# Kernel tuning notes

Measured on AMD Instinct MI355X. Metric: run time of the kernel, lower is better.

## Reference

```python
import jax, jax.numpy as jnp
import numpy as np

B, VL, TL, KL = 2, 2048, 448, 64  # batch, vision_len, text_len, task_len
H, NH, D = 1024, 16, 64           # hidden, num_heads, head_dim


def _linear(x, w, b):
    # torch nn.Linear convention: w is [out, in]
    return x @ w.T + b


def _attn(q, k, v):
    # q: [b, ql, n, d], k/v: [b, kl, n, d] -> [b, ql, n, d]
    d = q.shape[-1]
    scores = jnp.einsum('bqnd,bknd->bnqk', q, k) / d  # note: /d, not /sqrt(d), as in source
    probs = jax.nn.softmax(scores, axis=-1)
    return jnp.einsum('bnqk,bknd->bqnd', probs, v)


def setup_inputs() -> dict:
    key = jax.random.key(0)
    ks = jax.random.split(key, 20)
    s = 0.02
    inp = {
        'vision_hidden_states': jax.random.normal(ks[0], (B, VL, H), jnp.float32),
        'text_hidden_states': jax.random.normal(ks[1], (B, TL, H), jnp.float32),
        'task_hidden_states': jax.random.normal(ks[2], (B, KL, H), jnp.float32),
        'wq0': jax.random.normal(ks[3], (H, H), jnp.float32) * s,
        'bq0': jnp.zeros((H,), jnp.float32),
        'wk0': jax.random.normal(ks[4], (H, H), jnp.float32) * s,
        'bk0': jnp.zeros((H,), jnp.float32),
        'wv0': jax.random.normal(ks[5], (H, H), jnp.float32) * s,
        'bv0': jnp.zeros((H,), jnp.float32),
        'wq1': jax.random.normal(ks[6], (D, D), jnp.float32) * s,
        'bq1': jnp.zeros((D,), jnp.float32),
        'wk1': jax.random.normal(ks[7], (D, D), jnp.float32) * s,
        'bk1': jnp.zeros((D,), jnp.float32),
        'wv1': jax.random.normal(ks[8], (D, D), jnp.float32) * s,
        'bv1': jnp.zeros((D,), jnp.float32),
        'wo': jax.random.normal(ks[9], (H, H), jnp.float32) * s,
        'bo': jnp.zeros((H,), jnp.float32),
    }
    return inp


def reference(vision_hidden_states, text_hidden_states, task_hidden_states,
              wq0, bq0, wk0, bk0, wv0, bv0,
              wq1, bq1, wk1, bk1, wv1, bv1, wo, bo):
    b, vl, h = vision_hidden_states.shape
    tl = text_hidden_states.shape[1]
    kl = task_hidden_states.shape[1]
    total = vl + tl + kl

    hs = jnp.concatenate([vision_hidden_states, text_hidden_states, task_hidden_states], axis=1)
    q0 = _linear(hs, wq0, bq0).reshape(b, total, NH, D)
    k0 = _linear(hs, wk0, bk0).reshape(b, total, NH, D)
    v0 = _linear(hs, wv0, bv0).reshape(b, total, NH, D)

    vq, tq, kq = q0[:, :vl], q0[:, vl:vl + tl], q0[:, vl + tl:]
    vk, tk, kk = k0[:, :vl], k0[:, vl:vl + tl], k0[:, vl + tl:]
    vv, tv = v0[:, :vl], v0[:, vl:vl + tl]
    kv = q0[:, vl + tl:]  # faithful to source bug: task_v comes from q0

    v2t = _attn(vq, tk, tv)  # vision attends to text: [b, vl, n, d]
    t2v = _attn(tq, vk, vv)  # text attends to vision: [b, tl, n, d]
    mid = jnp.concatenate([v2t, t2v], axis=1)  # [b, vl+tl, n, d]

    q1 = jnp.concatenate([kq, _linear(mid, wq1, bq1)], axis=1)
    k1 = jnp.concatenate([kk, _linear(mid, wk1, bk1)], axis=1)
    v1 = jnp.concatenate([kv, _linear(mid, wv1, bv1)], axis=1)

    out = _attn(q1, k1, v1).reshape(b, total, NH * D)
    return _linear(out, wo, bo)
```

## Files before the change

### kernel.cpp

```cpp
#include <hip/hip_runtime.h>
#include <math.h>

#define NB   2
#define VL   2048
#define TL   448
#define KL   64
#define TOT  2560
#define MIDL 2496
#define HDIM 1024
#define NHEAD 16
#define DHEAD 64

typedef __bf16 bf16x8 __attribute__((ext_vector_type(8)));
typedef float  f32x4  __attribute__((ext_vector_type(4)));
typedef unsigned short us8 __attribute__((ext_vector_type(8)));
typedef float  fl4    __attribute__((ext_vector_type(4)));
typedef unsigned int u32x2 __attribute__((ext_vector_type(2)));

__device__ __forceinline__ unsigned short f2bf(float f) {
    unsigned int u = __builtin_bit_cast(unsigned int, f);
    u += 0x7FFFu + ((u >> 16) & 1u);
    return (unsigned short)(u >> 16);
}
__device__ __forceinline__ float bf2f(unsigned short u) {
    unsigned int x = ((unsigned int)u) << 16;
    return __builtin_bit_cast(float, x);
}
__device__ __forceinline__ f32x4 mfma_bf16(bf16x8 a, bf16x8 b, f32x4 c) {
    return __builtin_amdgcn_mfma_f32_16x16x32_bf16(a, b, c, 0, 0, 0);
}
__device__ __forceinline__ bf16x8 ldb(const unsigned short* p) {
    return __builtin_bit_cast(bf16x8, *(const us8*)p);
}

__global__ __launch_bounds__(256) void k_cast_hs(
    const float* __restrict__ vis, const float* __restrict__ txt,
    const float* __restrict__ tsk, unsigned short* __restrict__ X)
{
    size_t idx = ((size_t)blockIdx.x * 256 + threadIdx.x) * 4;
    if (idx >= (size_t)NB * TOT * HDIM) return;
    size_t r = idx >> 10; int c = (int)(idx & 1023);
    int b = (int)(r / TOT), s = (int)(r % TOT);
    const float* src;
    if (s < VL)        src = vis + ((size_t)b * VL + s) * HDIM;
    else if (s < MIDL) src = txt + ((size_t)b * TL + (s - VL)) * HDIM;
    else               src = tsk + ((size_t)b * KL + (s - MIDL)) * HDIM;
    fl4 v = *(const fl4*)(src + c);
    X[idx + 0] = f2bf(v[0]); X[idx + 1] = f2bf(v[1]);
    X[idx + 2] = f2bf(v[2]); X[idx + 3] = f2bf(v[3]);
}

__global__ __launch_bounds__(256) void k_cast(
    const float* __restrict__ in, unsigned short* __restrict__ out, int n)
{
    int idx = (blockIdx.x * 256 + threadIdx.x) * 4;
    if (idx >= n) return;
    fl4 v = *(const fl4*)(in + idx);
    out[idx + 0] = f2bf(v[0]); out[idx + 1] = f2bf(v[1]);
    out[idx + 2] = f2bf(v[2]); out[idx + 3] = f2bf(v[3]);
}

template<bool BF16OUT>
__global__ __launch_bounds__(256) void k_gemm_bt(
    const unsigned short* __restrict__ A, const unsigned short* __restrict__ W,
    const float* __restrict__ bias, void* __restrict__ Cv,
    int M, int N, int K)
{
    __shared__ unsigned short As[128][40];
    __shared__ unsigned short Bs[128][40];
    const int row0 = blockIdx.x * 128, col0 = blockIdx.y * 128;
    const int t = threadIdx.x;
    const int lane = t & 63, wave = t >> 6;
    const int wr = wave >> 1, wc = wave & 1;
    const int lrow = lane & 15, lgrp = lane >> 4;

    f32x4 acc[4][4];
    #pragma unroll
    for (int m = 0; m < 4; ++m)
        #pragma unroll
        for (int n = 0; n < 4; ++n)
            acc[m][n] = (f32x4){0.f, 0.f, 0.f, 0.f};

    const int r = t >> 1, hc = (t & 1) * 16;
    const unsigned short* Ap = A + (size_t)(row0 + r) * K + hc;
    const unsigned short* Wp = W + (size_t)(col0 + r) * K + hc;

    for (int kk = 0; kk < K; kk += 32) {
        us8 a0 = *(const us8*)(Ap + kk);
        us8 a1 = *(const us8*)(Ap + kk + 8);
        us8 b0 = *(const us8*)(Wp + kk);
        us8 b1 = *(const us8*)(Wp + kk + 8);
        __syncthreads();
        *(us8*)&As[r][hc]     = a0;
        *(us8*)&As[r][hc + 8] = a1;
        *(us8*)&Bs[r][hc]     = b0;
        *(us8*)&Bs[r][hc + 8] = b1;
        __syncthreads();
        bf16x8 af[4], bfr[4];
        #pragma unroll
        for (int m = 0; m < 4; ++m) af[m]  = ldb(&As[wr*64 + m*16 + lrow][lgrp*8]);
        #pragma unroll
        for (int n = 0; n < 4; ++n) bfr[n] = ldb(&Bs[wc*64 + n*16 + lrow][lgrp*8]);
        #pragma unroll
        for (int m = 0; m < 4; ++m)
            #pragma unroll
            for (int n = 0; n < 4; ++n)
                acc[m][n] = mfma_bf16(af[m], bfr[n], acc[m][n]);
    }
    #pragma unroll
    for (int m = 0; m < 4; ++m) {
        #pragma unroll
        for (int n = 0; n < 4; ++n) {
            int col = col0 + wc*64 + n*16 + lrow;
            float bs = bias[col];
            #pragma unroll
            for (int q = 0; q < 4; ++q) {
                int row = row0 + wr*64 + m*16 + lgrp*4 + q;
                float v = acc[m][n][q] + bs;
                if (BF16OUT) ((unsigned short*)Cv)[(size_t)row * N + col] = f2bf(v);
                else         ((float*)Cv)[(size_t)row * N + col] = v;
            }
        }
    }
}

__global__ __launch_bounds__(256) void k_gemm_qkv(
    const unsigned short* __restrict__ A, const unsigned short* __restrict__ W,
    const float* __restrict__ b0, const float* __restrict__ b1,
    const float* __restrict__ b2,
    unsigned short* __restrict__ C0, unsigned short* __restrict__ C1,
    unsigned short* __restrict__ C2)
{
    __shared__ unsigned short As[128][40];
    __shared__ unsigned short Bs[128][40];
    const int row0 = blockIdx.x * 128, col0 = blockIdx.y * 128;
    const int t = threadIdx.x;
    const int lane = t & 63, wave = t >> 6;
    const int wr = wave >> 1, wc = wave & 1;
    const int lrow = lane & 15, lgrp = lane >> 4;

    f32x4 acc[4][4];
    #pragma unroll
    for (int m = 0; m < 4; ++m)
        #pragma unroll
        for (int n = 0; n < 4; ++n)
            acc[m][n] = (f32x4){0.f, 0.f, 0.f, 0.f};

    const int r = t >> 1, hc = (t & 1) * 16;
    const unsigned short* Ap = A + (size_t)(row0 + r) * HDIM + hc;
    const unsigned short* Wp = W + (size_t)(col0 + r) * HDIM + hc;

    for (int kk = 0; kk < HDIM; kk += 32) {
        us8 a0 = *(const us8*)(Ap + kk);
        us8 a1 = *(const us8*)(Ap + kk + 8);
        us8 b0v = *(const us8*)(Wp + kk);
        us8 b1v = *(const us8*)(Wp + kk + 8);
        __syncthreads();
        *(us8*)&As[r][hc]     = a0;
        *(us8*)&As[r][hc + 8] = a1;
        *(us8*)&Bs[r][hc]     = b0v;
        *(us8*)&Bs[r][hc + 8] = b1v;
        __syncthreads();
        bf16x8 af[4], bfr[4];
        #pragma unroll
        for (int m = 0; m < 4; ++m) af[m]  = ldb(&As[wr*64 + m*16 + lrow][lgrp*8]);
        #pragma unroll
        for (int n = 0; n < 4; ++n) bfr[n] = ldb(&Bs[wc*64 + n*16 + lrow][lgrp*8]);
        #pragma unroll
        for (int m = 0; m < 4; ++m)
            #pragma unroll
            for (int n = 0; n < 4; ++n)
                acc[m][n] = mfma_bf16(af[m], bfr[n], acc[m][n]);
    }
    const int plane = col0 >> 10;
    const float* bp = (plane == 0) ? b0 : (plane == 1) ? b1 : b2;
    unsigned short* Cp = (plane == 0) ? C0 : (plane == 1) ? C1 : C2;
    const int cl0 = col0 & 1023;
    #pragma unroll
    for (int m = 0; m < 4; ++m) {
        #pragma unroll
        for (int n = 0; n < 4; ++n) {
            int col = cl0 + wc*64 + n*16 + lrow;
            float bs = bp[col];
            #pragma unroll
            for (int q = 0; q < 4; ++q) {
                int row = row0 + wr*64 + m*16 + lgrp*4 + q;
                Cp[(size_t)row * HDIM + col] = f2bf(acc[m][n][q] + bs);
            }
        }
    }
}

__global__ __launch_bounds__(256) void k_attn(
    const unsigned short* __restrict__ Qb, const unsigned short* __restrict__ Kb,
    const unsigned short* __restrict__ Vb, unsigned short* __restrict__ Ob,
    int Lk, size_t q_bs, size_t k_bs, size_t o_bs, float scale)
{
    __shared__ unsigned short QV[64 * 72];
    __shared__ unsigned short Ks[64][72];
    __shared__ unsigned short Pl[4][16][72];

    const int b = blockIdx.z, h = blockIdx.y, qb = blockIdx.x;
    const unsigned short* Q = Qb + (size_t)b * q_bs + h * 64;
    const unsigned short* K = Kb + (size_t)b * k_bs + h * 64;
    const unsigned short* V = Vb + (size_t)b * k_bs + h * 64;
    unsigned short*       O = Ob + (size_t)b * o_bs + h * 64;
    const int t = threadIdx.x;
    const int wave = t >> 6, lane = t & 63;
    const int lrow = lane & 15, lgrp = lane >> 4;
    const int q0r = qb * 64;

    #pragma unroll
    for (int i = 0; i < 2; ++i) {
        int c = t + i * 256, rr = c >> 3, off = (c & 7) * 8;
        *(us8*)&QV[rr*72 + off] = *(const us8*)(Q + (size_t)(q0r + rr) * HDIM + off);
    }
    __syncthreads();
    bf16x8 qf0 = ldb(&QV[(wave*16 + lrow)*72 + lgrp*8]);
    bf16x8 qf1 = ldb(&QV[(wave*16 + lrow)*72 + 32 + lgrp*8]);

    f32x4 oacc[4];
    #pragma unroll
    for (int d = 0; d < 4; ++d) oacc[d] = (f32x4){0.f, 0.f, 0.f, 0.f};
    float mr = -INFINITY;
    float lsum = 0.f;

    const int nkt = Lk >> 6;
    for (int kt = 0; kt < nkt; ++kt) {
        us8 kreg[2], vreg[2];
        #pragma unroll
        for (int i = 0; i < 2; ++i) {
            int c = t + i * 256, rr = c >> 3, off = (c & 7) * 8;
            kreg[i] = *(const us8*)(K + (size_t)(kt*64 + rr) * HDIM + off);
            vreg[i] = *(const us8*)(V + (size_t)(kt*64 + rr) * HDIM + off);
        }
        __syncthreads();
        #pragma unroll
        for (int i = 0; i < 2; ++i) {
            int c = t + i * 256, rr = c >> 3, off = (c & 7) * 8;
            *(us8*)&Ks[rr][off] = kreg[i];
            int colp = (((rr >> 3) ^ (off >> 3)) << 3) + (rr & 7);
            #pragma unroll
            for (int j = 0; j < 8; ++j)
                QV[(off + j)*72 + colp] = vreg[i][j];
        }
        __syncthreads();

        f32x4 s[4];
        #pragma unroll
        for (int nf = 0; nf < 4; ++nf) {
            bf16x8 kf0 = ldb(&Ks[nf*16 + lrow][lgrp*8]);
            bf16x8 kf1 = ldb(&Ks[nf*16 + lrow][32 + lgrp*8]);
            f32x4 z = (f32x4){0.f, 0.f, 0.f, 0.f};
            z = mfma_bf16(kf0, qf0, z);
            z = mfma_bf16(kf1, qf1, z);
            s[nf] = z * scale;
        }
        float mt = s[0][0];
        #pragma unroll
        for (int nf = 0; nf < 4; ++nf)
            #pragma unroll
            for (int r = 0; r < 4; ++r)
                mt = fmaxf(mt, s[nf][r]);
        mt = fmaxf(mt, __shfl_xor(mt, 16));
        mt = fmaxf(mt, __shfl_xor(mt, 32));
        float mn = fmaxf(mr, mt);
        float al = __expf(mr - mn);
        mr = mn;

        float rs = 0.f;
        #pragma unroll
        for (int nf = 0; nf < 4; ++nf) {
            unsigned short e0 = f2bf(__expf(s[nf][0] - mn));
            unsigned short e1 = f2bf(__expf(s[nf][1] - mn));
            unsigned short e2 = f2bf(__expf(s[nf][2] - mn));
            unsigned short e3 = f2bf(__expf(s[nf][3] - mn));
            rs += bf2f(e0) + bf2f(e1) + bf2f(e2) + bf2f(e3);
            u32x2 w;
            w[0] = (unsigned)e0 | ((unsigned)e1 << 16);
            w[1] = (unsigned)e2 | ((unsigned)e3 << 16);
            *(u32x2*)&Pl[wave][lrow][nf*16 + lgrp*4] = w;
        }
        rs += __shfl_xor(rs, 16);
        rs += __shfl_xor(rs, 32);
        lsum = lsum * al + rs;
        #pragma unroll
        for (int d = 0; d < 4; ++d) oacc[d] *= al;

        bf16x8 pb0 = ldb(&Pl[wave][lrow][lgrp*8]);
        bf16x8 pb1 = ldb(&Pl[wave][lrow][32 + lgrp*8]);
        #pragma unroll
        for (int df = 0; df < 4; ++df) {
            int d = df*16 + lrow;
            int f = (d >> 3) & 7;
            bf16x8 v0 = ldb(&QV[d*72 + ((lgrp ^ f) << 3)]);
            bf16x8 v1 = ldb(&QV[d*72 + (((4 | lgrp) ^ f) << 3)]);
            oacc[df] = mfma_bf16(v0, pb0, oacc[df]);
            oacc[df] = mfma_bf16(v1, pb1, oacc[df]);
        }
    }
    const float rcp = 1.0f / lsum;
    const int row = q0r + wave*16 + lrow;
    #pragma unroll
    for (int df = 0; df < 4; ++df) {
        unsigned short c0 = f2bf(oacc[df][0] * rcp);
        unsigned short c1 = f2bf(oacc[df][1] * rcp);
        unsigned short c2 = f2bf(oacc[df][2] * rcp);
        unsigned short c3 = f2bf(oacc[df][3] * rcp);
        u32x2 w;
        w[0] = (unsigned)c0 | ((unsigned)c1 << 16);
        w[1] = (unsigned)c2 | ((unsigned)c3 << 16);
        *(u32x2*)(O + (size_t)row * HDIM + df*16 + lgrp*4) = w;
    }
}

__global__ __launch_bounds__(256) void k_midlin(
    const unsigned short* __restrict__ mid,
    const unsigned short* __restrict__ wq, const unsigned short* __restrict__ wk,
    const unsigned short* __restrict__ wv,
    const float* __restrict__ bq, const float* __restrict__ bk,
    const float* __restrict__ bv,
    unsigned short* __restrict__ q1, unsigned short* __restrict__ k1,
    unsigned short* __restrict__ v1)
{
    __shared__ unsigned short As[128][72];
    const int r0 = blockIdx.x * 128, h = blockIdx.y;
    const int t = threadIdx.x;
    const int wave = t >> 6, lane = t & 63;
    const int lrow = lane & 15, lgrp = lane >> 4;

    #pragma unroll
    for (int i = 0; i < 4; ++i) {
        int c = t + i * 256, rr = c >> 3, off = (c & 7) * 8;
        *(us8*)&As[rr][off] = *(const us8*)(mid + (size_t)(r0 + rr) * HDIM + h*64 + off);
    }
    __syncthreads();
    bf16x8 af[2][2];
    #pragma unroll
    for (int m = 0; m < 2; ++m)
        #pragma unroll
        for (int kf = 0; kf < 2; ++kf)
            af[m][kf] = ldb(&As[wave*32 + m*16 + lrow][kf*32 + lgrp*8]);

    const unsigned short* ws[3] = {wq, wk, wv};
    const float* bs[3] = {bq, bk, bv};
    unsigned short* ds[3] = {q1, k1, v1};
    for (int o = 0; o < 3; ++o) {
        bf16x8 bfr[4][2];
        #pragma unroll
        for (int n = 0; n < 4; ++n)
            #pragma unroll
            for (int kf = 0; kf < 2; ++kf)
                bfr[n][kf] = __builtin_bit_cast(bf16x8,
                    *(const us8*)(ws[o] + (size_t)(n*16 + lrow) * 64 + kf*32 + lgrp*8));
        f32x4 acc[2][4];
        #pragma unroll
        for (int m = 0; m < 2; ++m)
            #pragma unroll
            for (int n = 0; n < 4; ++n) {
                f32x4 z = (f32x4){0.f, 0.f, 0.f, 0.f};
                z = mfma_bf16(af[m][0], bfr[n][0], z);
                z = mfma_bf16(af[m][1], bfr[n][1], z);
                acc[m][n] = z;
            }
        #pragma unroll
        for (int m = 0; m < 2; ++m)
            #pragma unroll
            for (int n = 0; n < 4; ++n) {
                float bb = bs[o][n*16 + lrow];
                #pragma unroll
                for (int q = 0; q < 4; ++q) {
                    int gr = r0 + wave*32 + m*16 + lgrp*4 + q;
                    int bi = gr / MIDL, seq = gr % MIDL;
                    size_t drow = (size_t)bi * TOT + 64 + seq;
                    ds[o][drow * HDIM + h*64 + n*16 + lrow] = f2bf(acc[m][n][q] + bb);
                }
            }
    }
}

__global__ __launch_bounds__(256) void k_copy_task(
    const unsigned short* __restrict__ q0, const unsigned short* __restrict__ k0,
    unsigned short* __restrict__ q1, unsigned short* __restrict__ k1,
    unsigned short* __restrict__ v1)
{
    int blk = blockIdx.x;
    int tensor = blk >> 7, rem = blk & 127;
    int b = rem >> 6, rr = rem & 63;
    const unsigned short* src = (tensor == 1) ? k0 : q0;
    unsigned short* dst = (tensor == 0) ? q1 : (tensor == 1 ? k1 : v1);
    size_t srow = (size_t)b * TOT + MIDL + rr;
    size_t drow = (size_t)b * TOT + rr;
    int t = threadIdx.x;
    if (t < 128)
        ((us8*)(dst + drow * HDIM))[t] = ((const us8*)(src + srow * HDIM))[t];
}

extern "C" void kernel_launch(void* const* d_in, const int* in_sizes, int n_in,
                              void* d_out, int out_size, void* d_ws, size_t ws_size,
                              hipStream_t stream)
{
    (void)in_sizes; (void)n_in; (void)out_size; (void)ws_size;
    const float* vis = (const float*)d_in[0];
    const float* txt = (const float*)d_in[1];
    const float* tsk = (const float*)d_in[2];
    const float* wq0 = (const float*)d_in[3];
    const float* bq0 = (const float*)d_in[4];
    const float* wk0 = (const float*)d_in[5];
    const float* bk0 = (const float*)d_in[6];
    const float* wv0 = (const float*)d_in[7];
    const float* bv0 = (const float*)d_in[8];
    const float* wq1 = (const float*)d_in[9];
    const float* bq1 = (const float*)d_in[10];
    const float* wk1 = (const float*)d_in[11];
    const float* bk1 = (const float*)d_in[12];
    const float* wv1 = (const float*)d_in[13];
    const float* bv1 = (const float*)d_in[14];
    const float* wo  = (const float*)d_in[15];
    const float* bo  = (const float*)d_in[16];

    char* ws = (char*)d_ws;
    size_t off = 0;
    auto carve = [&](size_t bytes) -> char* {
        char* p = ws + off;
        off += (bytes + 255) & ~(size_t)255;
        return p;
    };
    const size_t ELX = (size_t)NB * TOT * HDIM;
    unsigned short* X     = (unsigned short*)carve(ELX * 2);
    unsigned short* q0    = (unsigned short*)carve(ELX * 2);
    unsigned short* k0    = (unsigned short*)carve(ELX * 2);
    unsigned short* v0    = (unsigned short*)carve(ELX * 2);
    unsigned short* wqkvb = (unsigned short*)carve((size_t)3 * HDIM * HDIM * 2);
    unsigned short* wob   = (unsigned short*)carve((size_t)HDIM * HDIM * 2);
    unsigned short* wq1b  = (unsigned short*)carve(64 * 64 * 2);
    unsigned short* wk1b  = (unsigned short*)carve(64 * 64 * 2);
    unsigned short* wv1b  = (unsigned short*)carve(64 * 64 * 2);
    unsigned short* mid   = X;
    unsigned short* q1    = q0;
    unsigned short* k1    = k0;
    unsigned short* v1    = v0;
    unsigned short* out2  = X;

    const float scale = 1.0f / 64.0f;

    k_cast_hs<<<5120, 256, 0, stream>>>(vis, txt, tsk, X);
    k_cast<<<1024, 256, 0, stream>>>(wq0, wqkvb,                 HDIM * HDIM);
    k_cast<<<1024, 256, 0, stream>>>(wk0, wqkvb + 1024*1024,     HDIM * HDIM);
    k_cast<<<1024, 256, 0, stream>>>(wv0, wqkvb + 2*1024*1024,   HDIM * HDIM);
    k_cast<<<1024, 256, 0, stream>>>(wo,  wob,  HDIM * HDIM);
    k_cast<<<4, 256, 0, stream>>>(wq1, wq1b, 64 * 64);
    k_cast<<<4, 256, 0, stream>>>(wk1, wk1b, 64 * 64);
    k_cast<<<4, 256, 0, stream>>>(wv1, wv1b, 64 * 64);

    k_gemm_qkv<<<dim3(40, 24), 256, 0, stream>>>(
        X, wqkvb, bq0, bk0, bv0, q0, k0, v0);

    k_attn<<<dim3(VL/64, NHEAD, NB), 256, 0, stream>>>(
        q0, k0 + (size_t)VL * HDIM, v0 + (size_t)VL * HDIM, mid,
        TL, (size_t)TOT * HDIM, (size_t)TOT * HDIM, (size_t)MIDL * HDIM, scale);
    k_attn<<<dim3(TL/64, NHEAD, NB), 256, 0, stream>>>(
        q0 + (size_t)VL * HDIM, k0, v0, mid + (size_t)VL * HDIM,
        VL, (size_t)TOT * HDIM, (size_t)TOT * HDIM, (size_t)MIDL * HDIM, scale);

    k_copy_task<<<384, 256, 0, stream>>>(q0, k0, q1, k1, v1);
    k_midlin<<<dim3(39, NHEAD), 256, 0, stream>>>(
        mid, wq1b, wk1b, wv1b, bq1, bk1, bv1, q1, k1, v1);

    k_attn<<<dim3(TOT/64, NHEAD, NB), 256, 0, stream>>>(
        q1, k1, v1, out2,
        TOT, (size_t)TOT * HDIM, (size_t)TOT * HDIM, (size_t)TOT * HDIM, scale);

    k_gemm_bt<false><<<dim3(40, 8), 256, 0, stream>>>(out2, wob, bo, (float*)d_out,
                                                      NB*TOT, HDIM, HDIM);
}
```

Before: 429.6 us.

## Store V transposed per head so attention loads it directly without LDS transpose

The QKV GEMM, the mid-linear projection and the task copy now write V into a head-major transposed buffer [b,h,d,seq]. The attention kernel can then load V tiles with vector stores into shared memory instead of scattering eight scalar stores per element with a swizzle. The K/V global loads are also software-prefetched one tile ahead to overlap with compute. The cost is strided scattered 8-byte writes in the GEMM epilogues and a scalar transpose in the task-copy kernel, and there is a risk of bank conflicts on the now unswizzled V reads.

```diff
diff --git a/kernel.cpp b/kernel.cpp
--- a/kernel.cpp
+++ b/kernel.cpp
@@ -129,7 +129,7 @@
     const float* __restrict__ b0, const float* __restrict__ b1,
     const float* __restrict__ b2,
     unsigned short* __restrict__ C0, unsigned short* __restrict__ C1,
-    unsigned short* __restrict__ C2)
+    unsigned short* __restrict__ vT)
 {
     __shared__ unsigned short As[128][40];
     __shared__ unsigned short Bs[128][40];
@@ -173,28 +173,48 @@
                 acc[m][n] = mfma_bf16(af[m], bfr[n], acc[m][n]);
     }
     const int plane = col0 >> 10;
-    const float* bp = (plane == 0) ? b0 : (plane == 1) ? b1 : b2;
-    unsigned short* Cp = (plane == 0) ? C0 : (plane == 1) ? C1 : C2;
     const int cl0 = col0 & 1023;
-    #pragma unroll
-    for (int m = 0; m < 4; ++m) {
-        #pragma unroll
-        for (int n = 0; n < 4; ++n) {
-            int col = cl0 + wc*64 + n*16 + lrow;
-            float bs = bp[col];
-            #pragma unroll
-            for (int q = 0; q < 4; ++q) {
-                int row = row0 + wr*64 + m*16 + lgrp*4 + q;
-                Cp[(size_t)row * HDIM + col] = f2bf(acc[m][n][q] + bs);
+    if (plane < 2) {
+        const float* bp = (plane == 0) ? b0 : b1;
+        unsigned short* Cp = (plane == 0) ? C0 : C1;
+        #pragma unroll
+        for (int m = 0; m < 4; ++m)
+            #pragma unroll
+            for (int n = 0; n < 4; ++n) {
+                int col = cl0 + wc*64 + n*16 + lrow;
+                float bs = bp[col];
+                #pragma unroll
+                for (int q = 0; q < 4; ++q) {
+                    int row = row0 + wr*64 + m*16 + lgrp*4 + q;
+                    Cp[(size_t)row * HDIM + col] = f2bf(acc[m][n][q] + bs);
+                }
             }
-        }
+    } else {
+        #pragma unroll
+        for (int m = 0; m < 4; ++m)
+            #pragma unroll
+            for (int n = 0; n < 4; ++n) {
+                int col = cl0 + wc*64 + n*16 + lrow;
+                int hh = col >> 6, dd = col & 63;
+                float bs = b2[col];
+                int rowb = row0 + wr*64 + m*16 + lgrp*4;
+                int bb = rowb / TOT, sq = rowb % TOT;
+                unsigned short e0 = f2bf(acc[m][n][0] + bs);
+                unsigned short e1 = f2bf(acc[m][n][1] + bs);
+                unsigned short e2 = f2bf(acc[m][n][2] + bs);
+                unsigned short e3 = f2bf(acc[m][n][3] + bs);
+                u32x2 w;
+                w[0] = (unsigned)e0 | ((unsigned)e1 << 16);
+                w[1] = (unsigned)e2 | ((unsigned)e3 << 16);
+                *(u32x2*)(vT + ((size_t)(bb*NHEAD + hh)*64 + dd)*TOT + sq) = w;
+            }
     }
 }
 
 __global__ __launch_bounds__(256) void k_attn(
     const unsigned short* __restrict__ Qb, const unsigned short* __restrict__ Kb,
-    const unsigned short* __restrict__ Vb, unsigned short* __restrict__ Ob,
-    int Lk, size_t q_bs, size_t k_bs, size_t o_bs, float scale)
+    const unsigned short* __restrict__ vT, unsigned short* __restrict__ Ob,
+    int Lk, size_t q_bs, size_t k_bs, int v_seq0, size_t o_bs, float scale)
 {
     __shared__ unsigned short QV[64 * 72];
     __shared__ unsigned short Ks[64][72];
@@ -203,7 +223,7 @@
     const int b = blockIdx.z, h = blockIdx.y, qb = blockIdx.x;
     const unsigned short* Q = Qb + (size_t)b * q_bs + h * 64;
     const unsigned short* K = Kb + (size_t)b * k_bs + h * 64;
-    const unsigned short* V = Vb + (size_t)b * k_bs + h * 64;
+    const unsigned short* V = vT + ((size_t)(b*NHEAD + h) * 64) * TOT + v_seq0;
     unsigned short*       O = Ob + (size_t)b * o_bs + h * 64;
     const int t = threadIdx.x;
     const int wave = t >> 6, lane = t & 63;
@@ -225,24 +245,30 @@
     float mr = -INFINITY;
     float lsum = 0.f;
 
+    const int c0 = t,        rr0 = c0 >> 3, of0 = (c0 & 7) * 8;
+    const int c1 = t + 256,  rr1 = c1 >> 3, of1 = (c1 & 7) * 8;
+    const unsigned short* Kp0 = K + (size_t)rr0 * HDIM + of0;
+    const unsigned short* Kp1 = K + (size_t)rr1 * HDIM + of1;
+    const unsigned short* Vp0 = V + (size_t)rr0 * TOT + of0;
+    const unsigned short* Vp1 = V + (size_t)rr1 * TOT + of1;
+
     const int nkt = Lk >> 6;
+    us8 ka0 = *(const us8*)(Kp0);
+    us8 ka1 = *(const us8*)(Kp1);
+    us8 va0 = *(const us8*)(Vp0);
+    us8 va1 = *(const us8*)(Vp1);
+
     for (int kt = 0; kt < nkt; ++kt) {
-        us8 kreg[2], vreg[2];
-        #pragma unroll
-        for (int i = 0; i < 2; ++i) {
-            int c = t + i * 256, rr = c >> 3, off = (c & 7) * 8;
-            kreg[i] = *(const us8*)(K + (size_t)(kt*64 + rr) * HDIM + off);
-            vreg[i] = *(const us8*)(V + (size_t)(kt*64 + rr) * HDIM + off);
-        }
         __syncthreads();
-        #pragma unroll
-        for (int i = 0; i < 2; ++i) {
-            int c = t + i * 256, rr = c >> 3, off = (c & 7) * 8;
-            *(us8*)&Ks[rr][off] = kreg[i];
-            int colp = (((rr >> 3) ^ (off >> 3)) << 3) + (rr & 7);
-            #pragma unroll
-            for (int j = 0; j < 8; ++j)
-                QV[(off + j)*72 + colp] = vreg[i][j];
+        *(us8*)&Ks[rr0][of0] = ka0;
+        *(us8*)&Ks[rr1][of1] = ka1;
+        *(us8*)&QV[rr0*72 + of0] = va0;
+        *(us8*)&QV[rr1*72 + of1] = va1;
+        if (kt + 1 < nkt) {
+            ka0 = *(const us8*)(Kp0 + (size_t)(kt+1) * 64 * HDIM);
+            ka1 = *(const us8*)(Kp1 + (size_t)(kt+1) * 64 * HDIM);
+            va0 = *(const us8*)(Vp0 + (kt+1) * 64);
+            va1 = *(const us8*)(Vp1 + (kt+1) * 64);
         }
         __syncthreads();
 
@@ -260,8 +286,8 @@
         #pragma unroll
         for (int nf = 0; nf < 4; ++nf)
             #pragma unroll
-            for (int r = 0; r < 4; ++r)
-                mt = fmaxf(mt, s[nf][r]);
+            for (int rg = 0; rg < 4; ++rg)
+                mt = fmaxf(mt, s[nf][rg]);
         mt = fmaxf(mt, __shfl_xor(mt, 16));
         mt = fmaxf(mt, __shfl_xor(mt, 32));
         float mn = fmaxf(mr, mt);
@@ -292,9 +318,8 @@
         #pragma unroll
         for (int df = 0; df < 4; ++df) {
             int d = df*16 + lrow;
-            int f = (d >> 3) & 7;
-            bf16x8 v0 = ldb(&QV[d*72 + ((lgrp ^ f) << 3)]);
-            bf16x8 v1 = ldb(&QV[d*72 + (((4 | lgrp) ^ f) << 3)]);
+            bf16x8 v0 = ldb(&QV[d*72 + lgrp*8]);
+            bf16x8 v1 = ldb(&QV[d*72 + 32 + lgrp*8]);
             oacc[df] = mfma_bf16(v0, pb0, oacc[df]);
             oacc[df] = mfma_bf16(v1, pb1, oacc[df]);
         }
@@ -303,13 +328,13 @@
     const int row = q0r + wave*16 + lrow;
     #pragma unroll
     for (int df = 0; df < 4; ++df) {
-        unsigned short c0 = f2bf(oacc[df][0] * rcp);
-        unsigned short c1 = f2bf(oacc[df][1] * rcp);
-        unsigned short c2 = f2bf(oacc[df][2] * rcp);
-        unsigned short c3 = f2bf(oacc[df][3] * rcp);
+        unsigned short e0 = f2bf(oacc[df][0] * rcp);
+        unsigned short e1 = f2bf(oacc[df][1] * rcp);
+        unsigned short e2 = f2bf(oacc[df][2] * rcp);
+        unsigned short e3 = f2bf(oacc[df][3] * rcp);
         u32x2 w;
-        w[0] = (unsigned)c0 | ((unsigned)c1 << 16);
-        w[1] = (unsigned)c2 | ((unsigned)c3 << 16);
+        w[0] = (unsigned)e0 | ((unsigned)e1 << 16);
+        w[1] = (unsigned)e2 | ((unsigned)e3 << 16);
         *(u32x2*)(O + (size_t)row * HDIM + df*16 + lgrp*4) = w;
     }
 }
@@ -321,7 +346,7 @@
     const float* __restrict__ bq, const float* __restrict__ bk,
     const float* __restrict__ bv,
     unsigned short* __restrict__ q1, unsigned short* __restrict__ k1,
-    unsigned short* __restrict__ v1)
+    unsigned short* __restrict__ vT)
 {
     __shared__ unsigned short As[128][72];
     const int r0 = blockIdx.x * 128, h = blockIdx.y;
@@ -344,7 +369,8 @@
 
     const unsigned short* ws[3] = {wq, wk, wv};
     const float* bs[3] = {bq, bk, bv};
-    unsigned short* ds[3] = {q1, k1, v1};
+    unsigned short* ds[2] = {q1, k1};
+    #pragma unroll
     for (int o = 0; o < 3; ++o) {
         bf16x8 bfr[4][2];
         #pragma unroll
@@ -368,12 +394,26 @@
             #pragma unroll
             for (int n = 0; n < 4; ++n) {
                 float bb = bs[o][n*16 + lrow];
-                #pragma unroll
-                for (int q = 0; q < 4; ++q) {
-                    int gr = r0 + wave*32 + m*16 + lgrp*4 + q;
-                    int bi = gr / MIDL, seq = gr % MIDL;
-                    size_t drow = (size_t)bi * TOT + 64 + seq;
-                    ds[o][drow * HDIM + h*64 + n*16 + lrow] = f2bf(acc[m][n][q] + bb);
+                if (o < 2) {
+                    #pragma unroll
+                    for (int q = 0; q < 4; ++q) {
+                        int gr = r0 + wave*32 + m*16 + lgrp*4 + q;
+                        int bi = gr / MIDL, sq = gr % MIDL;
+                        size_t drow = (size_t)bi * TOT + 64 + sq;
+                        ds[o][drow * HDIM + h*64 + n*16 + lrow] = f2bf(acc[m][n][q] + bb);
+                    }
+                } else {
+                    int gr = r0 + wave*32 + m*16 + lgrp*4;
+                    int bi = gr / MIDL, sq = gr % MIDL;
+                    unsigned short e0 = f2bf(acc[m][n][0] + bb);
+                    unsigned short e1 = f2bf(acc[m][n][1] + bb);
+                    unsigned short e2 = f2bf(acc[m][n][2] + bb);
+                    unsigned short e3 = f2bf(acc[m][n][3] + bb);
+                    u32x2 w;
+                    w[0] = (unsigned)e0 | ((unsigned)e1 << 16);
+                    w[1] = (unsigned)e2 | ((unsigned)e3 << 16);
+                    *(u32x2*)(vT + ((size_t)(bi*NHEAD + h)*64 + (n*16+lrow))*TOT
+                              + 64 + sq) = w;
                 }
             }
     }
@@ -382,18 +422,31 @@
 __global__ __launch_bounds__(256) void k_copy_task(
     const unsigned short* __restrict__ q0, const unsigned short* __restrict__ k0,
     unsigned short* __restrict__ q1, unsigned short* __restrict__ k1,
-    unsigned short* __restrict__ v1)
+    unsigned short* __restrict__ vT)
 {
     int blk = blockIdx.x;
-    int tensor = blk >> 7, rem = blk & 127;
-    int b = rem >> 6, rr = rem & 63;
-    const unsigned short* src = (tensor == 1) ? k0 : q0;
-    unsigned short* dst = (tensor == 0) ? q1 : (tensor == 1 ? k1 : v1);
-    size_t srow = (size_t)b * TOT + MIDL + rr;
-    size_t drow = (size_t)b * TOT + rr;
     int t = threadIdx.x;
-    if (t < 128)
-        ((us8*)(dst + drow * HDIM))[t] = ((const us8*)(src + srow * HDIM))[t];
+    if (blk < 256) {
+        int tensor = blk >> 7, rem = blk & 127;
+        int b = rem >> 6, rr = rem & 63;
+        const unsigned short* src = tensor ? k0 : q0;
+        unsigned short* dst = tensor ? k1 : q1;
+        size_t srow = (size_t)b * TOT + MIDL + rr;
+        size_t drow = (size_t)b * TOT + rr;
+        if (t < 128)
+            ((us8*)(dst + drow * HDIM))[t] = ((const us8*)(src + srow * HDIM))[t];
+    } else {
+        int rem = blk - 256;
+        int b = rem >> 4, h = rem & 15;
+        const unsigned short* src = q0 + ((size_t)b * TOT + MIDL) * HDIM + h * 64;
+        unsigned short* dst = vT + ((size_t)(b*NHEAD + h) * 64) * TOT;
+        #pragma unroll
+        for (int i = 0; i < 16; ++i) {
+            int idx = t + i * 256;
+            int r = idx & 63, d = idx >> 6;
+            dst[(size_t)d * TOT + r] = src[(size_t)r * HDIM + d];
+        }
+    }
 }
 
 extern "C" void kernel_launch(void* const* d_in, const int* in_sizes, int n_in,
@@ -430,7 +483,7 @@
     unsigned short* X     = (unsigned short*)carve(ELX * 2);
     unsigned short* q0    = (unsigned short*)carve(ELX * 2);
     unsigned short* k0    = (unsigned short*)carve(ELX * 2);
-    unsigned short* v0    = (unsigned short*)carve(ELX * 2);
+    unsigned short* vT    = (unsigned short*)carve(ELX * 2);
     unsigned short* wqkvb = (unsigned short*)carve((size_t)3 * HDIM * HDIM * 2);
     unsigned short* wob   = (unsigned short*)carve((size_t)HDIM * HDIM * 2);
     unsigned short* wq1b  = (unsigned short*)carve(64 * 64 * 2);
@@ -439,7 +492,6 @@
     unsigned short* mid   = X;
     unsigned short* q1    = q0;
     unsigned short* k1    = k0;
-    unsigned short* v1    = v0;
     unsigned short* out2  = X;
 
     const float scale = 1.0f / 64.0f;
@@ -454,22 +506,22 @@
     k_cast<<<4, 256, 0, stream>>>(wv1, wv1b, 64 * 64);
 
     k_gemm_qkv<<<dim3(40, 24), 256, 0, stream>>>(
-        X, wqkvb, bq0, bk0, bv0, q0, k0, v0);
+        X, wqkvb, bq0, bk0, bv0, q0, k0, vT);
 
     k_attn<<<dim3(VL/64, NHEAD, NB), 256, 0, stream>>>(
-        q0, k0 + (size_t)VL * HDIM, v0 + (size_t)VL * HDIM, mid,
-        TL, (size_t)TOT * HDIM, (size_t)TOT * HDIM, (size_t)MIDL * HDIM, scale);
+        q0, k0 + (size_t)VL * HDIM, vT, mid,
+        TL, (size_t)TOT * HDIM, (size_t)TOT * HDIM, VL, (size_t)MIDL * HDIM, scale);
     k_attn<<<dim3(TL/64, NHEAD, NB), 256, 0, stream>>>(
-        q0 + (size_t)VL * HDIM, k0, v0, mid + (size_t)VL * HDIM,
-        VL, (size_t)TOT * HDIM, (size_t)TOT * HDIM, (size_t)MIDL * HDIM, scale);
-
-    k_copy_task<<<384, 256, 0, stream>>>(q0, k0, q1, k1, v1);
+        q0 + (size_t)VL * HDIM, k0, vT, mid + (size_t)VL * HDIM,
+        VL, (size_t)TOT * HDIM, (size_t)TOT * HDIM, 0, (size_t)MIDL * HDIM, scale);
+
+    k_copy_task<<<288, 256, 0, stream>>>(q0, k0, q1, k1, vT);
     k_midlin<<<dim3(39, NHEAD), 256, 0, stream>>>(
-        mid, wq1b, wk1b, wv1b, bq1, bk1, bv1, q1, k1, v1);
+        mid, wq1b, wk1b, wv1b, bq1, bk1, bv1, q1, k1, vT);
 
     k_attn<<<dim3(TOT/64, NHEAD, NB), 256, 0, stream>>>(
-        q1, k1, v1, out2,
-        TOT, (size_t)TOT * HDIM, (size_t)TOT * HDIM, (size_t)TOT * HDIM, scale);
+        q1, k1, vT, out2,
+        TOT, (size_t)TOT * HDIM, (size_t)TOT * HDIM, 0, (size_t)TOT * HDIM, scale);
 
     k_gemm_bt<false><<<dim3(40, 8), 256, 0, stream>>>(out2, wob, bo, (float*)d_out,
                                                       NB*TOT, HDIM, HDIM);
```

Result: faster. 411.0 us (-4.3%).
